# Kernel optimization log

Measured on AMD Instinct MI355X. Metric: run time of the kernel, lower is better.

## Reference

```python
import jax, jax.numpy as jnp
import numpy as np

N, INV, M, K, H = 131072, 256, 256, 64, 512
EPS = 1e-6  # rms norm eps
LN_EPS = 1e-5  # torch LayerNorm default


def setup_inputs() -> dict:
    key = jax.random.key(0)
    ks = jax.random.split(key, 12)
    r = lambda i, shp, s=1.0: jax.random.normal(ks[i], shp, jnp.float32) * s
    return {
        "atomic_embeddings": r(0, (N, INV + 3 * M)),
        "mean_inv": r(1, (INV,)) * 0.1,
        "std_inv": jax.random.uniform(ks[2], (INV,), jnp.float32, 0.5, 1.5),
        "rms_gamma": jnp.ones((M,), jnp.float32),
        "W0": r(3, (M, K)),
        "W1": r(4, (M, K)),
        "W2": r(5, (M, K)),
        "w_cross": r(6, (K, K)),
        "w_dot": r(7, (K, K)),
        "ln_w": jnp.ones((K,), jnp.float32),
        "ln_b": jnp.zeros((K,), jnp.float32),
        "g_w1": r(8, (INV, H)) / np.sqrt(INV),
        "g_b1": jnp.zeros((H,), jnp.float32),
        "g_w2": r(9, (H, K)) / np.sqrt(H),
        "g_b2": jnp.zeros((K,), jnp.float32),
    }


def reference(atomic_embeddings, mean_inv, std_inv, rms_gamma, W0, W1, W2,
              w_cross, w_dot, ln_w, ln_b, g_w1, g_b1, g_w2, g_b2):
    # split invariants (0e scalars come first) / equivariants (1o vectors)
    inv = atomic_embeddings[:, :INV]                       # [N, INV]
    eq = atomic_embeddings[:, INV:].reshape(-1, M, 3)      # [N, M, 3] e3nn (mul, ir) layout

    # rescale invariants
    inv = (inv - mean_inv) / std_inv

    # equivariant RMS layer norm over the M irrep channels (norm-based)
    n2 = jnp.sum(eq * eq, axis=-1)                          # [N, M] squared vector norms
    rms = jnp.sqrt(jnp.mean(n2, axis=-1, keepdims=True) + EPS)  # [N, 1]
    eq = eq * (rms_gamma / rms)[..., None]                  # [N, M, 3]

    # o3.Linear Mx1o -> Kx1o (per-component GEMM, e3nn 1/sqrt(fan_in) path norm)
    s_lin = 1.0 / np.sqrt(M)
    x0 = jnp.einsum('nmi,mk->nki', eq, W0) * s_lin          # [N, K, 3]
    x1 = jnp.einsum('nmi,mk->nki', eq, W1) * s_lin
    x2 = jnp.einsum('nmi,mk->nki', eq, W2) * s_lin

    # tp_cross: Kx1o (x) Kx1o -> Kx1e, 'uvu' weighted, component norm.
    # CG(1,1->1) = eps_ijk/sqrt(6); path weight sqrt(dim(1e)/fan_in)=sqrt(3/K)
    # => overall 1/sqrt(2K). Contract weight into x1 first to stay O(N K^2).
    y1 = jnp.einsum('nvj,uv->nuj', x1, w_cross)             # [N, K, 3]
    cross = jnp.cross(x0, y1) / np.sqrt(2.0 * K)            # [N, K, 3] (1e)

    # tp_dot: Kx1e (x) Kx1o -> Kx0o, 'uvu' weighted, component norm.
    # CG(1,1->0) = delta_ij/sqrt(3); path weight sqrt(1/K) => 1/sqrt(3K).
    y2 = jnp.einsum('nvj,uv->nuj', x2, w_dot)               # [N, K, 3]
    chi = jnp.sum(cross * y2, axis=-1) / np.sqrt(3.0 * K)   # [N, K] pseudoscalars

    # LayerNorm over K
    mu = jnp.mean(chi, axis=-1, keepdims=True)
    var = jnp.mean(jnp.square(chi - mu), axis=-1, keepdims=True)
    out = (chi - mu) / jnp.sqrt(var + LN_EPS) * ln_w + ln_b

    # ChiGate: sigmoid(Linear(SiLU(Linear(inv))))
    gate = jax.nn.sigmoid(jax.nn.silu(inv @ g_w1 + g_b1) @ g_w2 + g_b2)
    return gate * out
```

## Files before the change

kernel.cpp:

```cpp
#include <hip/hip_runtime.h>
#include <math.h>

#define ROW_D 1024
#define INV_D 256

typedef short bf16x8 __attribute__((ext_vector_type(8)));
typedef float f32x4 __attribute__((ext_vector_type(4)));

#define MFMA16(a,b,c) __builtin_amdgcn_mfma_f32_16x16x32_bf16((a),(b),(c),0,0,0)

__device__ __forceinline__ unsigned short f2bf(float f) {
    union { float f; unsigned int u; } x; x.f = f;
    return (unsigned short)((x.u + 0x7FFFu + ((x.u >> 16) & 1u)) >> 16);
}
__device__ __forceinline__ float bf2f(unsigned short h) {
    union { unsigned int u; float f; } x; x.u = ((unsigned int)h) << 16;
    return x.f;
}

__global__ void prep_kernel(
    const float* __restrict__ g_w1, const float* __restrict__ mean_inv,
    const float* __restrict__ std_inv, const float* __restrict__ g_w2,
    const float* __restrict__ W0, const float* __restrict__ W1,
    const float* __restrict__ W2, const float* __restrict__ rms_gamma,
    const float* __restrict__ w_cross, const float* __restrict__ w_dot,
    const float* __restrict__ g_b1,
    unsigned short* __restrict__ W1t, unsigned short* __restrict__ W2t,
    unsigned short* __restrict__ Wcat, unsigned short* __restrict__ wcb,
    unsigned short* __restrict__ wdb, float* __restrict__ b1p)
{
    const int nth = gridDim.x * 256;
    for (int idx = blockIdx.x * 256 + threadIdx.x; idx < 221696; idx += nth) {
        if (idx < 131072) {
            int h = idx >> 8, m = idx & 255;
            W1t[idx] = f2bf(g_w1[m * 512 + h] / std_inv[m]);
        } else if (idx < 163840) {
            int t = idx - 131072; int k = t >> 9, h = t & 511;
            W2t[t] = f2bf(g_w2[h * 64 + k]);
        } else if (idx < 212992) {
            int t = idx - 163840; int r = t >> 8, m = t & 255;
            int tt = r >> 6, k = r & 63;
            const float* Wt = (tt == 0) ? W0 : ((tt == 1) ? W1 : W2);
            Wcat[t] = f2bf(Wt[m * 64 + k] * rms_gamma[m] * 0.0625f);
        } else if (idx < 217088) {
            int t = idx - 212992; wcb[t] = f2bf(w_cross[t]);
        } else if (idx < 221184) {
            int t = idx - 217088; wdb[t] = f2bf(w_dot[t]);
        } else {
            int h = idx - 221184;
            float s = 0.f;
            for (int m = 0; m < 256; ++m)
                s += mean_inv[m] / std_inv[m] * g_w1[m * 512 + h];
            b1p[h] = g_b1[h] - s;
        }
    }
}

__global__ __launch_bounds__(256, 3) void gate_kernel(
    const float* __restrict__ emb,
    const unsigned short* __restrict__ W1t,
    const unsigned short* __restrict__ W2t,
    const float* __restrict__ b1p,
    const float* __restrict__ g_b2,
    float* __restrict__ out)
{
    __shared__ __align__(16) char smem[43008];
    unsigned short* As   = (unsigned short*)smem;
    unsigned short* acts = (unsigned short*)(smem + 33792);

    const int tid = threadIdx.x;
    const int wv = tid >> 6, ln = tid & 63;
    const int lr = ln & 15, lq = ln >> 4;
    const int wr = (wv & 1) << 1;
    const int wc = (wv >> 1) << 1;
    const long n0 = (long)blockIdx.x * 64;

#pragma unroll
    for (int i = 0; i < 16; ++i) {
        int idx = tid + i * 256;
        int atom = idx >> 6;
        int c4 = (idx & 63) << 2;
        float4 v = *(const float4*)(emb + (n0 + atom) * ROW_D + c4);
        ushort4 h;
        h.x = f2bf(v.x); h.y = f2bf(v.y); h.z = f2bf(v.z); h.w = f2bf(v.w);
        *(ushort4*)&As[atom * 264 + c4] = h;
    }
    __syncthreads();

    f32x4 acc2[2][2];
#pragma unroll
    for (int r = 0; r < 2; ++r)
#pragma unroll
        for (int c = 0; c < 2; ++c) acc2[r][c] = (f32x4){0.f, 0.f, 0.f, 0.f};

    for (int hc = 0; hc < 8; ++hc) {
        f32x4 acc1[2][2];
#pragma unroll
        for (int r = 0; r < 2; ++r)
#pragma unroll
            for (int c = 0; c < 2; ++c) acc1[r][c] = (f32x4){0.f, 0.f, 0.f, 0.f};

#pragma unroll
        for (int ks = 0; ks < 8; ++ks) {
            bf16x8 af[2], bf[2];
#pragma unroll
            for (int r = 0; r < 2; ++r)
                af[r] = *(const bf16x8*)&As[((wr + r) * 16 + lr) * 264 + ks * 32 + lq * 8];
#pragma unroll
            for (int c = 0; c < 2; ++c)
                bf[c] = *(const bf16x8*)(W1t + (hc * 64 + (wc + c) * 16 + lr) * 256
                                              + ks * 32 + lq * 8);
#pragma unroll
            for (int r = 0; r < 2; ++r)
#pragma unroll
                for (int c = 0; c < 2; ++c)
                    acc1[r][c] = MFMA16(af[r], bf[c], acc1[r][c]);
        }

#pragma unroll
        for (int c = 0; c < 2; ++c) {
            int hl = (wc + c) * 16 + lr;
            float b = b1p[hc * 64 + hl];
#pragma unroll
            for (int r = 0; r < 2; ++r)
#pragma unroll
                for (int g = 0; g < 4; ++g) {
                    int atom = (wr + r) * 16 + lq * 4 + g;
                    float v = acc1[r][c][g] + b;
                    acts[atom * 72 + hl] = f2bf(v / (1.f + __expf(-v)));
                }
        }
        __syncthreads();

#pragma unroll
        for (int ks = 0; ks < 2; ++ks) {
            bf16x8 af[2], bf[2];
#pragma unroll
            for (int r = 0; r < 2; ++r)
                af[r] = *(const bf16x8*)&acts[((wr + r) * 16 + lr) * 72 + ks * 32 + lq * 8];
#pragma unroll
            for (int c = 0; c < 2; ++c)
                bf[c] = *(const bf16x8*)(W2t + ((wc + c) * 16 + lr) * 512
                                              + hc * 64 + ks * 32 + lq * 8);
#pragma unroll
            for (int r = 0; r < 2; ++r)
#pragma unroll
                for (int c = 0; c < 2; ++c)
                    acc2[r][c] = MFMA16(af[r], bf[c], acc2[r][c]);
        }
        __syncthreads();
    }

#pragma unroll
    for (int c = 0; c < 2; ++c) {
        int k = (wc + c) * 16 + lr;
        float b2v = g_b2[k];
#pragma unroll
        for (int r = 0; r < 2; ++r)
#pragma unroll
            for (int g = 0; g < 4; ++g) {
                int atom = (wr + r) * 16 + lq * 4 + g;
                float v = acc2[r][c][g] + b2v;
                out[(n0 + atom) * 64 + k] = 1.f / (1.f + __expf(-v));
            }
    }
}

__global__ __launch_bounds__(256, 2) void chi_kernel(
    const float* __restrict__ emb,
    const unsigned short* __restrict__ Wcat,
    const unsigned short* __restrict__ wcb,
    const unsigned short* __restrict__ wdb,
    const float* __restrict__ ln_w,
    const float* __restrict__ ln_b,
    float* __restrict__ out)
{
    __shared__ __align__(16) char smem[62592];
    unsigned short* Aeq = (unsigned short*)smem;
    unsigned short* Bw  = (unsigned short*)(smem + 13824);
    unsigned short* Xl1 = (unsigned short*)smem;
    unsigned short* Xl2 = (unsigned short*)(smem + 13824);
    unsigned short* y1l = (unsigned short*)smem;
    unsigned short* y2l = (unsigned short*)(smem + 13824);
    unsigned short* x0l = (unsigned short*)(smem + 41472);
    float* chi_s = (float*)(smem + 54016);
    float* rms_s = (float*)(smem + 62464);

    const int tid = threadIdx.x;
    const int wv = tid >> 6, ln = tid & 63;
    const int lr = ln & 15, lq = ln >> 4;
    const int a_t = tid >> 3, st = tid & 7;
    const long n0 = (long)blockIdx.x * 32;

    f32x4 acc[6][3];
#pragma unroll
    for (int tr = 0; tr < 6; ++tr)
#pragma unroll
        for (int c = 0; c < 3; ++c) acc[tr][c] = (f32x4){0.f, 0.f, 0.f, 0.f};
    float sumsq = 0.f;

    for (int kb = 0; kb < 4; ++kb) {
        __syncthreads();
#pragma unroll
        for (int j = 0; j < 6; ++j) {
            int c = (st + 8 * j) * 4;
            float4 v = *(const float4*)(emb + (n0 + a_t) * ROW_D + INV_D + kb * 192 + c);
            sumsq += v.x * v.x + v.y * v.y + v.z * v.z + v.w * v.w;
            float vv[4] = {v.x, v.y, v.z, v.w};
#pragma unroll
            for (int e = 0; e < 4; ++e) {
                int col = c + e;
                int ml = col / 3;
                int ii = col - ml * 3;
                Aeq[(ii * 32 + a_t) * 72 + ml] = f2bf(vv[e]);
            }
        }
#pragma unroll
        for (int i = 0; i < 6; ++i) {
            int idx = tid + i * 256;
            int row = idx >> 3, c8 = (idx & 7) << 3;
            *(uint4*)&Bw[row * 72 + c8] =
                *(const uint4*)(Wcat + row * 256 + kb * 64 + c8);
        }
        __syncthreads();
#pragma unroll
        for (int ks = 0; ks < 2; ++ks) {
            bf16x8 bfr[3];
#pragma unroll
            for (int c = 0; c < 3; ++c)
                bfr[c] = *(const bf16x8*)&Bw[((wv * 3 + c) * 16 + lr) * 72 + ks * 32 + lq * 8];
#pragma unroll
            for (int tr = 0; tr < 6; ++tr) {
                bf16x8 af = *(const bf16x8*)&Aeq[(tr * 16 + lr) * 72 + ks * 32 + lq * 8];
#pragma unroll
                for (int c = 0; c < 3; ++c)
                    acc[tr][c] = MFMA16(af, bfr[c], acc[tr][c]);
            }
        }
    }
    sumsq += __shfl_xor(sumsq, 1);
    sumsq += __shfl_xor(sumsq, 2);
    sumsq += __shfl_xor(sumsq, 4);
    if (st == 0) rms_s[a_t] = rsqrtf(sumsq * (1.f / 256.f) + 1e-6f);
    __syncthreads();

#pragma unroll
    for (int tr = 0; tr < 6; ++tr)
#pragma unroll
        for (int c = 0; c < 3; ++c) {
            int colg = (wv * 3 + c) * 16 + lr;
            int t = colg >> 6, k = colg & 63;
#pragma unroll
            for (int g = 0; g < 4; ++g) {
                int rowg = tr * 16 + lq * 4 + g;
                int ii = rowg >> 5, atom = rowg & 31;
                unsigned short hb = f2bf(acc[tr][c][g] * rms_s[atom]);
                if (t == 0)      x0l[atom * 196 + k * 3 + ii] = hb;
                else if (t == 1) Xl1[(atom * 3 + ii) * 72 + k] = hb;
                else             Xl2[(atom * 3 + ii) * 72 + k] = hb;
            }
        }
    __syncthreads();

    const int ts = wv & 1, cp = wv >> 1;
    const unsigned short* Xs = ts ? Xl2 : Xl1;
    const unsigned short* Wg = ts ? wdb : wcb;
    f32x4 yacc[6][2];
#pragma unroll
    for (int tr = 0; tr < 6; ++tr)
#pragma unroll
        for (int c = 0; c < 2; ++c) yacc[tr][c] = (f32x4){0.f, 0.f, 0.f, 0.f};
#pragma unroll
    for (int ks = 0; ks < 2; ++ks) {
        bf16x8 bfr[2];
#pragma unroll
        for (int c = 0; c < 2; ++c)
            bfr[c] = *(const bf16x8*)(Wg + ((cp * 2 + c) * 16 + lr) * 64 + ks * 32 + lq * 8);
#pragma unroll
        for (int tr = 0; tr < 6; ++tr) {
            bf16x8 af = *(const bf16x8*)&Xs[(tr * 16 + lr) * 72 + ks * 32 + lq * 8];
#pragma unroll
            for (int c = 0; c < 2; ++c)
                yacc[tr][c] = MFMA16(af, bfr[c], yacc[tr][c]);
        }
    }
    __syncthreads();

    unsigned short* Yd = ts ? y2l : y1l;
#pragma unroll
    for (int tr = 0; tr < 6; ++tr)
#pragma unroll
        for (int c = 0; c < 2; ++c) {
            int u = (cp * 2 + c) * 16 + lr;
#pragma unroll
            for (int g = 0; g < 4; ++g) {
                int rowg = tr * 16 + lq * 4 + g;
                Yd[rowg * 72 + u] = f2bf(yacc[tr][c][g]);
            }
        }
    __syncthreads();

    const float CHI_SCALE = 1.0f / sqrtf(24576.0f);
#pragma unroll
    for (int q = 0; q < 8; ++q) {
        int u = st + 8 * q;
        float x0a = bf2f(x0l[a_t * 196 + u * 3 + 0]);
        float x0b = bf2f(x0l[a_t * 196 + u * 3 + 1]);
        float x0c = bf2f(x0l[a_t * 196 + u * 3 + 2]);
        float y1a = bf2f(y1l[(a_t * 3 + 0) * 72 + u]);
        float y1b = bf2f(y1l[(a_t * 3 + 1) * 72 + u]);
        float y1c = bf2f(y1l[(a_t * 3 + 2) * 72 + u]);
        float y2a = bf2f(y2l[(a_t * 3 + 0) * 72 + u]);
        float y2b = bf2f(y2l[(a_t * 3 + 1) * 72 + u]);
        float y2c = bf2f(y2l[(a_t * 3 + 2) * 72 + u]);
        float c0 = x0b * y1c - x0c * y1b;
        float c1 = x0c * y1a - x0a * y1c;
        float c2 = x0a * y1b - x0b * y1a;
        chi_s[a_t * 66 + u] = (c0 * y2a + c1 * y2b + c2 * y2c) * CHI_SCALE;
    }
    __syncthreads();

    float s = 0.f;
#pragma unroll
    for (int q = 0; q < 8; ++q) s += chi_s[a_t * 66 + st + 8 * q];
    s += __shfl_xor(s, 1); s += __shfl_xor(s, 2); s += __shfl_xor(s, 4);
    float mu = s * (1.f / 64.f);
    float vv = 0.f;
#pragma unroll
    for (int q = 0; q < 8; ++q) {
        float d = chi_s[a_t * 66 + st + 8 * q] - mu;
        vv += d * d;
    }
    vv += __shfl_xor(vv, 1); vv += __shfl_xor(vv, 2); vv += __shfl_xor(vv, 4);
    float isd = rsqrtf(vv * (1.f / 64.f) + 1e-5f);
#pragma unroll
    for (int q = 0; q < 8; ++q) {
        int u = st + 8 * q;
        float val = (chi_s[a_t * 66 + u] - mu) * isd * ln_w[u] + ln_b[u];
        long o = (n0 + a_t) * 64 + u;
        out[o] = out[o] * val;
    }
}

extern "C" void kernel_launch(void* const* d_in, const int* in_sizes, int n_in,
                              void* d_out, int out_size, void* d_ws, size_t ws_size,
                              hipStream_t stream)
{
    const float* emb       = (const float*)d_in[0];
    const float* mean_inv  = (const float*)d_in[1];
    const float* std_inv   = (const float*)d_in[2];
    const float* rms_gamma = (const float*)d_in[3];
    const float* W0        = (const float*)d_in[4];
    const float* W1        = (const float*)d_in[5];
    const float* W2        = (const float*)d_in[6];
    const float* w_cross   = (const float*)d_in[7];
    const float* w_dot     = (const float*)d_in[8];
    const float* ln_w      = (const float*)d_in[9];
    const float* ln_b      = (const float*)d_in[10];
    const float* g_w1      = (const float*)d_in[11];
    const float* g_b1      = (const float*)d_in[12];
    const float* g_w2      = (const float*)d_in[13];
    const float* g_b2      = (const float*)d_in[14];
    float* out = (float*)d_out;

    char* ws = (char*)d_ws;
    unsigned short* W1t  = (unsigned short*)(ws);
    unsigned short* W2t  = (unsigned short*)(ws + 262144);
    unsigned short* Wcat = (unsigned short*)(ws + 327680);
    unsigned short* wcb  = (unsigned short*)(ws + 425984);
    unsigned short* wdb  = (unsigned short*)(ws + 434176);
    float*          b1p  = (float*)(ws + 442368);

    const int N = in_sizes[0] / ROW_D;

    prep_kernel<<<128, 256, 0, stream>>>(g_w1, mean_inv, std_inv, g_w2,
                                         W0, W1, W2, rms_gamma, w_cross, w_dot,
                                         g_b1, W1t, W2t, Wcat, wcb, wdb, b1p);
    gate_kernel<<<N / 64, 256, 0, stream>>>(emb, W1t, W2t, b1p, g_b2, out);
    chi_kernel<<<N / 32, 256, 0, stream>>>(emb, Wcat, wcb, wdb, ln_w, ln_b, out);
}
```

Measured before the change: 955.5 us.

## Cut chi_kernel LDS, read weights from global, coalesce loads and output

The weight tile is no longer staged in shared memory; B fragments are read directly from global/L2. The equivariant input is loaded as full atoms in two halves, with each load split into three components and written as vectorized ushort4. Shared memory drops enough to allow three blocks per CU, and the launch bounds are raised to match. The final LayerNorm/gate multiply is reorganized so each wave writes contiguous 64-float rows, at the cost of an extra barrier and more global weight reads per block.

```diff
diff --git a/kernel.cpp b/kernel.cpp
--- a/kernel.cpp
+++ b/kernel.cpp
@@ -166,7 +166,7 @@
     }
 }
 
-__global__ __launch_bounds__(256, 2) void chi_kernel(
+__global__ __launch_bounds__(256, 3) void chi_kernel(
     const float* __restrict__ emb,
     const unsigned short* __restrict__ Wcat,
     const unsigned short* __restrict__ wcb,
@@ -175,16 +175,17 @@
     const float* __restrict__ ln_b,
     float* __restrict__ out)
 {
-    __shared__ __align__(16) char smem[62592];
+    __shared__ __align__(16) char smem[49024];
     unsigned short* Aeq = (unsigned short*)smem;
-    unsigned short* Bw  = (unsigned short*)(smem + 13824);
     unsigned short* Xl1 = (unsigned short*)smem;
     unsigned short* Xl2 = (unsigned short*)(smem + 13824);
     unsigned short* y1l = (unsigned short*)smem;
     unsigned short* y2l = (unsigned short*)(smem + 13824);
-    unsigned short* x0l = (unsigned short*)(smem + 41472);
-    float* chi_s = (float*)(smem + 54016);
-    float* rms_s = (float*)(smem + 62464);
+    unsigned short* x0l = (unsigned short*)(smem + 27648);
+    float* chi_s = (float*)(smem + 40192);
+    float* rms_s = (float*)(smem + 48640);
+    float* mu_s  = (float*)(smem + 48768);
+    float* isd_s = (float*)(smem + 48896);
 
     const int tid = threadIdx.x;
     const int wv = tid >> 6, ln = tid & 63;
@@ -199,39 +200,38 @@
         for (int c = 0; c < 3; ++c) acc[tr][c] = (f32x4){0.f, 0.f, 0.f, 0.f};
     float sumsq = 0.f;
 
-    for (int kb = 0; kb < 4; ++kb) {
+    for (int half = 0; half < 2; ++half) {
+        if (half) __syncthreads();
+#pragma unroll
+        for (int g = 0; g < 4; ++g) {
+            int m0 = st * 16 + g * 4;
+            int mg = half * 128 + m0;
+            const float* p = emb + (n0 + a_t) * ROW_D + INV_D + (long)mg * 3;
+            float4 v0 = *(const float4*)(p);
+            float4 v1 = *(const float4*)(p + 4);
+            float4 v2 = *(const float4*)(p + 8);
+            sumsq += v0.x * v0.x + v0.y * v0.y + v0.z * v0.z + v0.w * v0.w
+                   + v1.x * v1.x + v1.y * v1.y + v1.z * v1.z + v1.w * v1.w
+                   + v2.x * v2.x + v2.y * v2.y + v2.z * v2.z + v2.w * v2.w;
+            ushort4 h0, h1, h2;
+            h0.x = f2bf(v0.x); h0.y = f2bf(v0.w); h0.z = f2bf(v1.z); h0.w = f2bf(v2.y);
+            h1.x = f2bf(v0.y); h1.y = f2bf(v1.x); h1.z = f2bf(v1.w); h1.w = f2bf(v2.z);
+            h2.x = f2bf(v0.z); h2.y = f2bf(v1.y); h2.z = f2bf(v2.x); h2.w = f2bf(v2.w);
+            *(ushort4*)&Aeq[(0 * 32 + a_t) * 136 + m0] = h0;
+            *(ushort4*)&Aeq[(1 * 32 + a_t) * 136 + m0] = h1;
+            *(ushort4*)&Aeq[(2 * 32 + a_t) * 136 + m0] = h2;
+        }
         __syncthreads();
 #pragma unroll
-        for (int j = 0; j < 6; ++j) {
-            int c = (st + 8 * j) * 4;
-            float4 v = *(const float4*)(emb + (n0 + a_t) * ROW_D + INV_D + kb * 192 + c);
-            sumsq += v.x * v.x + v.y * v.y + v.z * v.z + v.w * v.w;
-            float vv[4] = {v.x, v.y, v.z, v.w};
-#pragma unroll
-            for (int e = 0; e < 4; ++e) {
-                int col = c + e;
-                int ml = col / 3;
-                int ii = col - ml * 3;
-                Aeq[(ii * 32 + a_t) * 72 + ml] = f2bf(vv[e]);
-            }
-        }
-#pragma unroll
-        for (int i = 0; i < 6; ++i) {
-            int idx = tid + i * 256;
-            int row = idx >> 3, c8 = (idx & 7) << 3;
-            *(uint4*)&Bw[row * 72 + c8] =
-                *(const uint4*)(Wcat + row * 256 + kb * 64 + c8);
-        }
-        __syncthreads();
-#pragma unroll
-        for (int ks = 0; ks < 2; ++ks) {
+        for (int ks = 0; ks < 4; ++ks) {
             bf16x8 bfr[3];
 #pragma unroll
             for (int c = 0; c < 3; ++c)
-                bfr[c] = *(const bf16x8*)&Bw[((wv * 3 + c) * 16 + lr) * 72 + ks * 32 + lq * 8];
+                bfr[c] = *(const bf16x8*)(Wcat + ((wv * 3 + c) * 16 + lr) * 256
+                                               + half * 128 + ks * 32 + lq * 8);
 #pragma unroll
             for (int tr = 0; tr < 6; ++tr) {
-                bf16x8 af = *(const bf16x8*)&Aeq[(tr * 16 + lr) * 72 + ks * 32 + lq * 8];
+                bf16x8 af = *(const bf16x8*)&Aeq[(tr * 16 + lr) * 136 + ks * 32 + lq * 8];
 #pragma unroll
                 for (int c = 0; c < 3; ++c)
                     acc[tr][c] = MFMA16(af, bfr[c], acc[tr][c]);
@@ -244,6 +244,12 @@
     if (st == 0) rms_s[a_t] = rsqrtf(sumsq * (1.f / 256.f) + 1e-6f);
     __syncthreads();
 
+    float rmv[2][4];
+#pragma unroll
+    for (int p = 0; p < 2; ++p)
+#pragma unroll
+        for (int g = 0; g < 4; ++g) rmv[p][g] = rms_s[p * 16 + lq * 4 + g];
+
 #pragma unroll
     for (int tr = 0; tr < 6; ++tr)
 #pragma unroll
@@ -254,7 +260,7 @@
             for (int g = 0; g < 4; ++g) {
                 int rowg = tr * 16 + lq * 4 + g;
                 int ii = rowg >> 5, atom = rowg & 31;
-                unsigned short hb = f2bf(acc[tr][c][g] * rms_s[atom]);
+                unsigned short hb = f2bf(acc[tr][c][g] * rmv[tr & 1][g]);
                 if (t == 0)      x0l[atom * 196 + k * 3 + ii] = hb;
                 else if (t == 1) Xl1[(atom * 3 + ii) * 72 + k] = hb;
                 else             Xl2[(atom * 3 + ii) * 72 + k] = hb;
@@ -332,12 +338,18 @@
         vv += d * d;
     }
     vv += __shfl_xor(vv, 1); vv += __shfl_xor(vv, 2); vv += __shfl_xor(vv, 4);
-    float isd = rsqrtf(vv * (1.f / 64.f) + 1e-5f);
-#pragma unroll
-    for (int q = 0; q < 8; ++q) {
-        int u = st + 8 * q;
-        float val = (chi_s[a_t * 66 + u] - mu) * isd * ln_w[u] + ln_b[u];
-        long o = (n0 + a_t) * 64 + u;
+    if (st == 0) {
+        mu_s[a_t]  = mu;
+        isd_s[a_t] = rsqrtf(vv * (1.f / 64.f) + 1e-5f);
+    }
+    __syncthreads();
+
+    float lw = ln_w[ln], lb = ln_b[ln];
+#pragma unroll
+    for (int aa = 0; aa < 8; ++aa) {
+        int atom = wv * 8 + aa;
+        float val = (chi_s[atom * 66 + ln] - mu_s[atom]) * isd_s[atom] * lw + lb;
+        long o = (n0 + atom) * 64 + ln;
         out[o] = out[o] * val;
     }
 }
```

Result: no change. 970.4 us (+1.6%).
